# Performance work log

Measured on AMD Instinct MI355X. Metric: run time of the kernel, lower is better.

Reference implementation:

```python
import jax, jax.numpy as jnp
import numpy as np

SXY_BF, SC_BF = 70.0, 12.0
COMPAT_BF, COMPAT_SPATIAL = 4.0, 2.0
SXY_SPATIAL = 6
NUM_ITER = 5
N_OUT = 21


def _gkern_depthwise(std, chans):
    # matches gkern(): sig_sq even -> r = sig_sq - 1, s = 2r+1
    sig_sq = std ** 2
    r = sig_sq if sig_sq % 2 else sig_sq - 1
    s = 2 * r + 1
    yy, xx = np.meshgrid(np.arange(s), np.arange(s), indexing='ij')
    k = np.exp(-(((yy - r) ** 2 + (xx - r) ** 2) / (2.0 * sig_sq)))
    k = k / k.sum()
    # original builds a [C,C,s,s] diagonal kernel == depthwise [C,1,s,s]
    return jnp.asarray(np.broadcast_to(k[None, None], (chans, 1, s, s)).copy(), jnp.float32)


def setup_inputs() -> dict:
    key = jax.random.key(0)
    k1, k2 = jax.random.split(key)
    unary = jax.random.uniform(k1, (2, N_OUT, 64, 64), dtype=jnp.float32)
    ref = jax.random.uniform(k2, (2, 3, 64, 64), dtype=jnp.float32) * 255.0  # RGB image
    gk = _gkern_depthwise(SXY_SPATIAL, N_OUT)
    kstd = jnp.asarray([SXY_BF, SXY_BF, SC_BF, SC_BF, SC_BF], jnp.float32)
    return {"unary": unary, "ref": ref, "gk": gk, "kstd": kstd}


def _crf_forward(unary, ref, gk, kstd):
    N, C, H, W = unary.shape
    P = H * W
    # stacked reference features: [y, x, r, g, b]
    yy, xx = jnp.meshgrid(jnp.arange(H, dtype=jnp.float32),
                          jnp.arange(W, dtype=jnp.float32), indexing='ij')
    grid = jnp.broadcast_to(jnp.stack([yy, xx])[None], (N, 2, H, W))
    stacked = jnp.concatenate([grid, ref], axis=1)  # [N,5,H,W]
    feats = (stacked / kstd[None, :, None, None]).reshape(N, -1, P).transpose(0, 2, 1)  # [N,P,5]
    # exact dense Gaussian (bilateral) kernel: K[p,q] = exp(-||f_p - f_q||^2 / 2)
    sq = jnp.sum(feats * feats, axis=-1)  # [N,P]
    d2 = sq[:, :, None] + sq[:, None, :] - 2.0 * jnp.einsum('npd,nqd->npq', feats, feats)
    K = jnp.exp(-0.5 * jnp.maximum(d2, 0.0))  # [N,P,P]

    U = jnp.log(jnp.clip(unary, 1e-5, 1.0))
    q = jax.nn.softmax(U, axis=1)
    pad = gk.shape[-1] // 2
    for i in range(NUM_ITER):
        qbf = jnp.einsum('npq,ncq->ncp', K, q.reshape(N, C, P)).reshape(N, C, H, W)
        qsf = jax.lax.conv_general_dilated(
            q, gk, window_strides=(1, 1), padding=[(pad, pad), (pad, pad)],
            feature_group_count=C, dimension_numbers=('NCHW', 'OIHW', 'NCHW'))
        q_hat = U + COMPAT_BF * qbf + COMPAT_SPATIAL * qsf
        q = jax.nn.softmax(q_hat, axis=1)  # normalize_final_iter=True
    return q


def reference(unary, ref, gk, kstd):
    return _crf_forward(unary, ref, gk, kstd)
```

## Files before the change

kernel.cpp:

```cpp
#include <hip/hip_runtime.h>
#include <math.h>

#ifndef __has_builtin
#define __has_builtin(x) 0
#endif
#if __has_builtin(__builtin_amdgcn_exp2f)
#define EXP2F(x) __builtin_amdgcn_exp2f(x)
#else
#define EXP2F(x) exp2f(x)
#endif

#define L2E  1.44269504088896340736f
#define RL2E 0.69314718055994530942f

#define NBATCH 2
#define NC 21
#define NP 4096
#define KR 35
#define NUM_ITER 5

typedef _Float16 half_t;
typedef _Float16 h8 __attribute__((ext_vector_type(8)));
typedef _Float16 h4 __attribute__((ext_vector_type(4)));
typedef float f4 __attribute__((ext_vector_type(4)));
typedef float f2 __attribute__((ext_vector_type(2)));
#define MFMA16(a, b, c) __builtin_amdgcn_mfma_f32_16x16x32_f16((a), (b), (c), 0, 0, 0)

static __device__ __forceinline__ f2 pk_fma(f2 a, f2 b, f2 c) {
    f2 d;
    asm volatile("v_pk_fma_f32 %0, %1, %2, %3" : "=v"(d) : "v"(a), "v"(b), "v"(c));
    return d;
}
static __device__ __forceinline__ f2 pk_add(f2 a, f2 b) {
    f2 d;
    asm volatile("v_pk_add_f32 %0, %1, %2" : "=v"(d) : "v"(a), "v"(b));
    return d;
}

#define PTILE 128
#define NPT   32
#define SQ    16
#define CHUNK 256
#define STEPS 8
#define NBBIL (NBATCH * NPT * SQ)
#define NBCONV (NBATCH * NC)
#define SEG_HALVES 256

#define OFF_QFEAT 0
#define OFF_QSOA  65536
#define OFF_UT    114688
#define OFF_QSF   311296
#define OFF_G     483328
#define OFF_QH16  485376
#define OFF_PART  845824
#define OFF_KMAT  2942976

#define LDS_BYTES 27648
#define QLS_STRIDE 264

__global__ __launch_bounds__(256) void setup_kernel(
    const float* __restrict__ unary, const float* __restrict__ ref,
    const float* __restrict__ kstd, float* __restrict__ ws,
    float* __restrict__ outq)
{
    int gid = blockIdx.x * 256 + threadIdx.x;
    if (gid < 4096) {
        float s = 0.f;
        for (int t = -KR; t <= KR; ++t) s += expf(-(float)(t * t) * (1.0f / 72.0f));
        int y = gid >> 6, yp = gid & 63;
        int d = y - yp;
        float v = (d >= -KR && d <= KR) ? expf(-(float)(d * d) * (1.0f / 72.0f)) / s : 0.f;
        ((half_t*)(ws + OFF_G))[gid] = (half_t)v;
    }
    if (gid >= NBATCH * NP) return;
    int n = gid >> 12, p = gid & (NP - 1);
    int y = p >> 6, x = p & 63;
    float k0 = kstd[0], k1 = kstd[1], k2 = kstd[2], k3 = kstd[3], k4 = kstd[4];
    const float* rp = ref + n * 3 * NP + p;
    float f0 = (float)y / k0;
    float f1 = (float)x / k1;
    float f2_ = rp[0]      / k2;
    float f3 = rp[NP]     / k3;
    float f4_ = rp[2 * NP] / k4;
    float sq = f0*f0 + f1*f1 + f2_*f2_ + f3*f3 + f4_*f4_;
    float h  = -0.5f * L2E * sq;
    float* qf = ws + OFF_QFEAT + gid * 8;
    qf[0]=L2E*f0; qf[1]=L2E*f1; qf[2]=L2E*f2_; qf[3]=L2E*f3; qf[4]=L2E*f4_;
    qf[5]=h; qf[6]=0.f; qf[7]=0.f;
    float* qs = ws + OFF_QSOA;
    qs[0*8192 + gid] = L2E*f0;  qs[1*8192 + gid] = L2E*f1;
    qs[2*8192 + gid] = L2E*f2_; qs[3*8192 + gid] = L2E*f3;
    qs[4*8192 + gid] = L2E*f4_; qs[5*8192 + gid] = h;

    float U[NC], e[NC];
    const float* up = unary + n * NC * NP + p;
    float m = -1e30f;
    for (int c = 0; c < NC; ++c) {
        float u = up[c * NP];
        u = fminf(fmaxf(u, 1e-5f), 1.0f);
        U[c] = logf(u);
        m = fmaxf(m, U[c]);
    }
    float ssum = 0.f;
    for (int c = 0; c < NC; ++c) { e[c] = EXP2F(L2E * (U[c] - m)); ssum += e[c]; }
    float inv = 1.0f / ssum;
    float* ut = ws + OFF_UT + gid * 24;
    half_t* qh = (half_t*)(ws + OFF_QH16);
    for (int c = 0; c < NC; ++c) {
        float qv = e[c] * inv;
        ut[c] = U[c];
        qh[(n * 24 + c) * NP + p] = (half_t)qv;
        outq[(n * NC + c) * NP + p] = qv;
    }
    ut[21] = 0.f; ut[22] = 0.f; ut[23] = 0.f;
    qh[(n * 24 + 21) * NP + p] = (half_t)0.f;
    qh[(n * 24 + 22) * NP + p] = (half_t)0.f;
    qh[(n * 24 + 23) * NP + p] = (half_t)0.f;
}

__global__ __launch_bounds__(256) void bilat_conv_kernel(
    const float* __restrict__ qfeatA,
    const float* __restrict__ qsoa,
    const half_t* __restrict__ qh16,
    const half_t* __restrict__ gmat,
    half_t* __restrict__ part,
    float* __restrict__ qsf,
    half_t* __restrict__ kmat,
    int first)
{
    __shared__ __align__(16) char lds[LDS_BYTES];
    int b = blockIdx.x;
    int tid = threadIdx.x;
    int l = tid & 63, w = tid >> 6;

    if (b < NBBIL) {
        int n  = b & 1;
        int pt = (b >> 1) & (NPT - 1);
        int s  = b >> 6;
        float*  qsoaS = (float*)lds;
        half_t* qls   = (half_t*)(lds + 6144);

        if (first) {
            for (int i = tid; i < 6 * (CHUNK / 4); i += 256) {
                int d = i >> 6, g = i & 63;
                *(f4*)(qsoaS + d * CHUNK + g * 4) =
                    *(const f4*)(qsoa + (size_t)d * 8192 + n * NP + s * CHUNK + g * 4);
            }
        }
        for (int i = tid; i < 21 * (CHUNK / 8); i += 256) {
            int c = i >> 5, g = i & 31;
            *(h8*)(qls + c * QLS_STRIDE + g * 8) =
                *(const h8*)(qh16 + (size_t)(n * 24 + c) * NP + s * CHUNK + g * 8);
        }
        for (int i = tid; i < 11 * 33; i += 256) {
            int c = 21 + i / 33, g = i % 33;
            *(h8*)(qls + c * QLS_STRIDE + g * 8) = (h8)(half_t)0.f;
        }
        half_t* kbase = kmat + (size_t)((b * 4 + w) * 2) * 8 * 512 + (size_t)l * 8;

        f4 acc[2][2];
        #pragma unroll
        for (int mt = 0; mt < 2; ++mt) { acc[mt][0] = (f4)0.f; acc[mt][1] = (f4)0.f; }
        int kq = (l >> 4) * 8;

        if (first) {
            f2 pf2[2][5], ph2[2];
            #pragma unroll
            for (int mt = 0; mt < 2; ++mt) {
                const float* fp = qfeatA + (size_t)(n * NP + pt * PTILE + (w * 2 + mt) * 16 + (l & 15)) * 8;
                #pragma unroll
                for (int i = 0; i < 5; ++i) {
                    float v = fp[i] * RL2E;
                    pf2[mt][i] = (f2){v, v};
                }
                ph2[mt] = (f2){fp[5], fp[5]};
            }
            __syncthreads();

            for (int step = 0; step < STEPS; ++step) {
                int qbase = step * 32 + kq;
                h8 kv[2];
                #pragma unroll
                for (int hf = 0; hf < 2; ++hf) {
                    f4 qf0 = *(const f4*)(qsoaS + 0 * CHUNK + qbase + hf * 4);
                    f4 qf1 = *(const f4*)(qsoaS + 1 * CHUNK + qbase + hf * 4);
                    f4 qf2 = *(const f4*)(qsoaS + 2 * CHUNK + qbase + hf * 4);
                    f4 qf3 = *(const f4*)(qsoaS + 3 * CHUNK + qbase + hf * 4);
                    f4 qf4 = *(const f4*)(qsoaS + 4 * CHUNK + qbase + hf * 4);
                    f4 qf5 = *(const f4*)(qsoaS + 5 * CHUNK + qbase + hf * 4);
                    #pragma unroll
                    for (int pr = 0; pr < 2; ++pr) {
                        f2 q0 = {qf0[2*pr], qf0[2*pr+1]};
                        f2 q1 = {qf1[2*pr], qf1[2*pr+1]};
                        f2 q2 = {qf2[2*pr], qf2[2*pr+1]};
                        f2 q3 = {qf3[2*pr], qf3[2*pr+1]};
                        f2 q4 = {qf4[2*pr], qf4[2*pr+1]};
                        f2 qh2 = {qf5[2*pr], qf5[2*pr+1]};
                        #pragma unroll
                        for (int mt = 0; mt < 2; ++mt) {
                            f2 e = pk_add(qh2, ph2[mt]);
                            e = pk_fma(pf2[mt][0], q0, e);
                            e = pk_fma(pf2[mt][1], q1, e);
                            e = pk_fma(pf2[mt][2], q2, e);
                            e = pk_fma(pf2[mt][3], q3, e);
                            e = pk_fma(pf2[mt][4], q4, e);
                            kv[mt][hf * 4 + pr * 2]     = (half_t)EXP2F(e[0]);
                            kv[mt][hf * 4 + pr * 2 + 1] = (half_t)EXP2F(e[1]);
                        }
                    }
                }
                *(h8*)(kbase + (size_t)(0 * 8 + step) * 512) = kv[0];
                *(h8*)(kbase + (size_t)(1 * 8 + step) * 512) = kv[1];

                h8 bf0 = *(const h8*)(qls + (size_t)(l & 15) * QLS_STRIDE + qbase);
                h8 bf1 = *(const h8*)(qls + (size_t)(16 + (l & 15)) * QLS_STRIDE + qbase);
                #pragma unroll
                for (int mt = 0; mt < 2; ++mt) {
                    acc[mt][0] = MFMA16(kv[mt], bf0, acc[mt][0]);
                    acc[mt][1] = MFMA16(kv[mt], bf1, acc[mt][1]);
                }
            }
        } else {
            __syncthreads();
            #pragma unroll
            for (int step = 0; step < STEPS; ++step) {
                int qbase = step * 32 + kq;
                h8 kv0 = *(const h8*)(kbase + (size_t)(0 * 8 + step) * 512);
                h8 kv1 = *(const h8*)(kbase + (size_t)(1 * 8 + step) * 512);
                h8 bf0 = *(const h8*)(qls + (size_t)(l & 15) * QLS_STRIDE + qbase);
                h8 bf1 = *(const h8*)(qls + (size_t)(16 + (l & 15)) * QLS_STRIDE + qbase);
                acc[0][0] = MFMA16(kv0, bf0, acc[0][0]);
                acc[0][1] = MFMA16(kv0, bf1, acc[0][1]);
                acc[1][0] = MFMA16(kv1, bf0, acc[1][0]);
                acc[1][1] = MFMA16(kv1, bf1, acc[1][1]);
            }
        }
        #pragma unroll
        for (int mt = 0; mt < 2; ++mt) {
            #pragma unroll
            for (int cht = 0; cht < 2; ++cht) {
                int segFlat = ((((s * 2 + n) * NPT + pt) * 4 + w) * 2 + mt) * 2 + cht;
                h4 hv;
                hv[0] = (half_t)acc[mt][cht][0];
                hv[1] = (half_t)acc[mt][cht][1];
                hv[2] = (half_t)acc[mt][cht][2];
                hv[3] = (half_t)acc[mt][cht][3];
                *(h4*)(part + (size_t)segFlat * SEG_HALVES + l * 4) = hv;
            }
        }
    } else {
        int cb = b - NBBIL;
        int n = cb / NC, c = cb % NC;
        half_t* qt = (half_t*)lds;
        half_t* gl = (half_t*)(lds + 9216);
        half_t* dl = (half_t*)(lds + 18432);

        for (int i = tid; i < 512; i += 256) {
            int row = i >> 3, g = i & 7;
            *(h8*)(gl + row * 72 + g * 8) = *(const h8*)(gmat + row * 64 + g * 8);
        }
        const half_t* qsrc = qh16 + (size_t)(n * 24 + c) * NP;
        for (int i = tid; i < 512; i += 256) {
            int row = i >> 3, g = i & 7;
            h8 v = *(const h8*)(qsrc + row * 64 + g * 8);
            #pragma unroll
            for (int k = 0; k < 8; ++k) qt[(g * 8 + k) * 72 + row] = v[k];
        }
        __syncthreads();

        int m0 = w * 16;
        f4 acc1[4];
        #pragma unroll
        for (int nt = 0; nt < 4; ++nt) acc1[nt] = (f4)0.f;
        #pragma unroll
        for (int ks = 0; ks < 2; ++ks) {
            h8 af = *(const h8*)(gl + (size_t)(m0 + (l & 15)) * 72 + ks * 32 + (l >> 4) * 8);
            #pragma unroll
            for (int nt = 0; nt < 4; ++nt) {
                h8 bf = *(const h8*)(qt + (size_t)(nt * 16 + (l & 15)) * 72 + ks * 32 + (l >> 4) * 8);
                acc1[nt] = MFMA16(af, bf, acc1[nt]);
            }
        }
        #pragma unroll
        for (int nt = 0; nt < 4; ++nt)
            #pragma unroll
            for (int r = 0; r < 4; ++r)
                dl[(size_t)(m0 + (l >> 4) * 4 + r) * 72 + nt * 16 + (l & 15)] = (half_t)acc1[nt][r];
        __syncthreads();

        f4 acc2[4];
        #pragma unroll
        for (int nt = 0; nt < 4; ++nt) acc2[nt] = (f4)0.f;
        #pragma unroll
        for (int ks = 0; ks < 2; ++ks) {
            h8 af = *(const h8*)(dl + (size_t)(m0 + (l & 15)) * 72 + ks * 32 + (l >> 4) * 8);
            #pragma unroll
            for (int nt = 0; nt < 4; ++nt) {
                h8 bf = *(const h8*)(gl + (size_t)(nt * 16 + (l & 15)) * 72 + ks * 32 + (l >> 4) * 8);
                acc2[nt] = MFMA16(af, bf, acc2[nt]);
            }
        }
        float* dst = qsf + (size_t)(n * NC + c) * NP;
        #pragma unroll
        for (int nt = 0; nt < 4; ++nt)
            #pragma unroll
            for (int r = 0; r < 4; ++r)
                dst[(size_t)(m0 + (l >> 4) * 4 + r) * 64 + nt * 16 + (l & 15)] = acc2[nt][r];
    }
}

__global__ __launch_bounds__(256) void reduce_update_kernel(
    const half_t* __restrict__ part, const float* __restrict__ ut_,
    const float* __restrict__ qsf, float* __restrict__ outq,
    half_t* __restrict__ qh16, int last)
{
    __shared__ float red[1024];
    int rb = blockIdx.x;
    int tid = threadIdx.x;
    int n = rb & 1, pt = (rb >> 1) & 31, wq = rb >> 6;
    int lseg = tid >> 6, l = tid & 63;

    float a0 = 0.f, a1 = 0.f, a2 = 0.f, a3 = 0.f;
    for (int s = 0; s < SQ; ++s) {
        size_t segF = (size_t)((((s * 2 + n) * NPT + pt) * 4 + wq) * 4 + lseg);
        h4 v = *(const h4*)(part + segF * SEG_HALVES + (size_t)l * 4);
        a0 += (float)v[0]; a1 += (float)v[1]; a2 += (float)v[2]; a3 += (float)v[3];
    }
    *(f4*)(red + tid * 4) = (f4){a0, a1, a2, a3};
    __syncthreads();

    if (tid < 32) {
        int pp = tid;
        int p = pt * PTILE + wq * 32 + pp;
        int gid = n * NP + p;
        int mtl = pp >> 4, mrow = pp & 15;
        int lg2 = mrow >> 2, reg = mrow & 3;

        const float* ut = ut_ + (size_t)gid * 24;
        const float* qs = qsf + (size_t)n * NC * NP + p;
        float e[NC];
        float m = -1e30f;
        #pragma unroll
        for (int c = 0; c < NC; ++c) {
            int cht = c >> 4, chL = c & 15;
            float qb = red[(mtl * 2 + cht) * 256 + (lg2 * 16 + chL) * 4 + reg];
            float li = ut[c] + 4.0f * qb + 2.0f * qs[c * NP];
            e[c] = li;
            m = fmaxf(m, li);
        }
        float ssum = 0.f;
        #pragma unroll
        for (int c = 0; c < NC; ++c) { float v = EXP2F(L2E * (e[c] - m)); e[c] = v; ssum += v; }
        float inv = 1.0f / ssum;
        if (last) {
            #pragma unroll
            for (int c = 0; c < NC; ++c)
                outq[(size_t)(n * NC + c) * NP + p] = e[c] * inv;
        } else {
            #pragma unroll
            for (int c = 0; c < NC; ++c)
                qh16[(size_t)(n * 24 + c) * NP + p] = (half_t)(e[c] * inv);
        }
    }
}

extern "C" void kernel_launch(void* const* d_in, const int* in_sizes, int n_in,
                              void* d_out, int out_size, void* d_ws, size_t ws_size,
                              hipStream_t stream)
{
    const float* unary = (const float*)d_in[0];
    const float* ref   = (const float*)d_in[1];
    const float* kstd  = (const float*)d_in[3];
    float* ws   = (float*)d_ws;
    float* outq = (float*)d_out;

    const float*  qfeatA = ws + OFF_QFEAT;
    const float*  qsoa   = ws + OFF_QSOA;
    float*        ut     = ws + OFF_UT;
    float*        qsf    = ws + OFF_QSF;
    const half_t* gmat   = (const half_t*)(ws + OFF_G);
    half_t*       qh16   = (half_t*)(ws + OFF_QH16);
    half_t*       part   = (half_t*)(ws + OFF_PART);
    half_t*       kmat   = (half_t*)(ws + OFF_KMAT);

    setup_kernel<<<32, 256, 0, stream>>>(unary, ref, kstd, ws, outq);
    for (int it = 0; it < NUM_ITER; ++it) {
        bilat_conv_kernel<<<NBBIL + NBCONV, 256, 0, stream>>>(
            qfeatA, qsoa, qh16, gmat, part, qsf, kmat, it == 0 ? 1 : 0);
        reduce_update_kernel<<<256, 256, 0, stream>>>(
            part, ut, qsf, outq, qh16, it == NUM_ITER - 1 ? 1 : 0);
    }
}
```

Measured before the change: 159.2 us.

## Fold spatial Gaussian into combined dense kernel and fuse reduction into one iteration kernel

Folds the separable spatial Gaussian convolution into the dense bilateral matrix, so each stored kernel entry holds 4*K_bf + 2*G_spatial. The conv blocks and the separate partial-sum reduction kernel go away. Each block now owns 32 pixels across all 4096 columns, with 512 threads and double-buffered LDS chunks, and reduces across waves in LDS before doing the softmax. This cuts launches from two per iteration to one and removes the fp16 partial round trip. The cost is less parallelism, since only 256 blocks each loop 16 chunks serially. The combined values are also stored in fp16, which may cost precision.

```diff
diff --git a/kernel.cpp b/kernel.cpp
--- a/kernel.cpp
+++ b/kernel.cpp
@@ -12,16 +12,17 @@
 
 #define L2E  1.44269504088896340736f
 #define RL2E 0.69314718055994530942f
+#define GEXPC (-L2E / 72.0f)
 
 #define NBATCH 2
 #define NC 21
 #define NP 4096
 #define KR 35
 #define NUM_ITER 5
+#define CHUNK 256
 
 typedef _Float16 half_t;
 typedef _Float16 h8 __attribute__((ext_vector_type(8)));
-typedef _Float16 h4 __attribute__((ext_vector_type(4)));
 typedef float f4 __attribute__((ext_vector_type(4)));
 typedef float f2 __attribute__((ext_vector_type(2)));
 #define MFMA16(a, b, c) __builtin_amdgcn_mfma_f32_16x16x32_f16((a), (b), (c), 0, 0, 0)
@@ -37,40 +38,25 @@
     return d;
 }
 
-#define PTILE 128
-#define NPT   32
-#define SQ    16
-#define CHUNK 256
-#define STEPS 8
-#define NBBIL (NBATCH * NPT * SQ)
-#define NBCONV (NBATCH * NC)
-#define SEG_HALVES 256
-
 #define OFF_QFEAT 0
 #define OFF_QSOA  65536
 #define OFF_UT    114688
-#define OFF_QSF   311296
-#define OFF_G     483328
-#define OFF_QH16  485376
-#define OFF_PART  845824
-#define OFF_KMAT  2942976
-
-#define LDS_BYTES 27648
+#define OFF_QA    311296
+#define OFF_QB    409600
+#define OFF_G     507904
+#define OFF_KMAT  524288
+
 #define QLS_STRIDE 264
 
 __global__ __launch_bounds__(256) void setup_kernel(
     const float* __restrict__ unary, const float* __restrict__ ref,
-    const float* __restrict__ kstd, float* __restrict__ ws,
-    float* __restrict__ outq)
+    const float* __restrict__ kstd, float* __restrict__ ws)
 {
     int gid = blockIdx.x * 256 + threadIdx.x;
-    if (gid < 4096) {
+    if (gid == 0) {
         float s = 0.f;
         for (int t = -KR; t <= KR; ++t) s += expf(-(float)(t * t) * (1.0f / 72.0f));
-        int y = gid >> 6, yp = gid & 63;
-        int d = y - yp;
-        float v = (d >= -KR && d <= KR) ? expf(-(float)(d * d) * (1.0f / 72.0f)) / s : 0.f;
-        ((half_t*)(ws + OFF_G))[gid] = (half_t)v;
+        ws[OFF_G] = 1.0f - 2.0f * log2f(s);
     }
     if (gid >= NBATCH * NP) return;
     int n = gid >> 12, p = gid & (NP - 1);
@@ -105,252 +91,208 @@
     for (int c = 0; c < NC; ++c) { e[c] = EXP2F(L2E * (U[c] - m)); ssum += e[c]; }
     float inv = 1.0f / ssum;
     float* ut = ws + OFF_UT + gid * 24;
-    half_t* qh = (half_t*)(ws + OFF_QH16);
+    half_t* qh = (half_t*)(ws + OFF_QA);
     for (int c = 0; c < NC; ++c) {
         float qv = e[c] * inv;
         ut[c] = U[c];
         qh[(n * 24 + c) * NP + p] = (half_t)qv;
-        outq[(n * NC + c) * NP + p] = qv;
-    }
-    ut[21] = 0.f; ut[22] = 0.f; ut[23] = 0.f;
-    qh[(n * 24 + 21) * NP + p] = (half_t)0.f;
-    qh[(n * 24 + 22) * NP + p] = (half_t)0.f;
-    qh[(n * 24 + 23) * NP + p] = (half_t)0.f;
-}
-
-__global__ __launch_bounds__(256) void bilat_conv_kernel(
+    }
+}
+
+__global__ __launch_bounds__(512) void crf_iter_kernel(
     const float* __restrict__ qfeatA,
     const float* __restrict__ qsoa,
-    const half_t* __restrict__ qh16,
-    const half_t* __restrict__ gmat,
-    half_t* __restrict__ part,
-    float* __restrict__ qsf,
+    const half_t* __restrict__ qin,
+    half_t* __restrict__ qout,
+    const float* __restrict__ ut_,
     half_t* __restrict__ kmat,
-    int first)
+    float* __restrict__ outq,
+    const float* __restrict__ gconst,
+    int first, int last)
 {
-    __shared__ __align__(16) char lds[LDS_BYTES];
+    __shared__ __align__(16) char lds[46080];
+    half_t* qlsA = (half_t*)lds;
+    half_t* qlsB = (half_t*)(lds + 16896);
+    float*  qsoA = (float*)(lds + 33792);
+    float*  qsoB = (float*)(lds + 39936);
+
     int b = blockIdx.x;
+    int n = b & 1, ptA = b >> 1;
     int tid = threadIdx.x;
-    int l = tid & 63, w = tid >> 6;
-
-    if (b < NBBIL) {
-        int n  = b & 1;
-        int pt = (b >> 1) & (NPT - 1);
-        int s  = b >> 6;
-        float*  qsoaS = (float*)lds;
-        half_t* qls   = (half_t*)(lds + 6144);
-
+    int l = tid & 63, v = tid >> 6;
+    int kq = (l >> 4) * 8;
+    int qoff = v * 32 + kq;
+
+    for (int i = tid; i < 2 * 363; i += 512) {
+        int bi = (i >= 363);
+        int j = i - bi * 363;
+        int c = 21 + j / 33, g = j % 33;
+        half_t* q = bi ? qlsB : qlsA;
+        *(h8*)(q + c * QLS_STRIDE + g * 8) = (h8)(half_t)0.f;
+    }
+    for (int i = tid; i < 672; i += 512) {
+        int c = i >> 5, g = i & 31;
+        *(h8*)(qlsA + c * QLS_STRIDE + g * 8) =
+            *(const h8*)(qin + (size_t)(n * 24 + c) * NP + g * 8);
+    }
+    if (first) {
+        for (int i = tid; i < 384; i += 512) {
+            int d = i >> 6, g = i & 63;
+            *(f4*)(qsoA + d * CHUNK + g * 4) =
+                *(const f4*)(qsoa + (size_t)d * 8192 + n * NP + g * 4);
+        }
+    }
+
+    f2 pf2[2][5], ph2[2];
+    int yp[2] = {0, 0}, xp[2] = {0, 0};
+    float C2p1 = 0.f;
+    if (first) {
+        C2p1 = gconst[0];
+        #pragma unroll
+        for (int mt = 0; mt < 2; ++mt) {
+            int pp = ptA * 32 + mt * 16 + (l & 15);
+            const float* fp = qfeatA + (size_t)(n * NP + pp) * 8;
+            #pragma unroll
+            for (int i = 0; i < 5; ++i) { float vv = fp[i] * RL2E; pf2[mt][i] = (f2){vv, vv}; }
+            ph2[mt] = (f2){fp[5], fp[5]};
+            yp[mt] = pp >> 6; xp[mt] = pp & 63;
+        }
+    }
+
+    f4 acc[2][2];
+    acc[0][0] = (f4)0.f; acc[0][1] = (f4)0.f;
+    acc[1][0] = (f4)0.f; acc[1][1] = (f4)0.f;
+
+    size_t fb = (size_t)b * (16 * 16 * 512);
+    h8 kv0 = (h8)(half_t)0.f, kv1 = (h8)(half_t)0.f;
+    if (!first) {
+        kv0 = *(const h8*)(kmat + fb + (size_t)(v * 2 + 0) * 512 + l * 8);
+        kv1 = *(const h8*)(kmat + fb + (size_t)(v * 2 + 1) * 512 + l * 8);
+    }
+    __syncthreads();
+
+    for (int s = 0; s < 16; ++s) {
+        half_t* qc = (s & 1) ? qlsB : qlsA;
+        half_t* qn = (s & 1) ? qlsA : qlsB;
+        float*  sc = (s & 1) ? qsoB : qsoA;
+        float*  sn = (s & 1) ? qsoA : qsoB;
+
+        if (s < 15) {
+            for (int i = tid; i < 672; i += 512) {
+                int c = i >> 5, g = i & 31;
+                *(h8*)(qn + c * QLS_STRIDE + g * 8) =
+                    *(const h8*)(qin + (size_t)(n * 24 + c) * NP + (s + 1) * CHUNK + g * 8);
+            }
+            if (first) {
+                for (int i = tid; i < 384; i += 512) {
+                    int d = i >> 6, g = i & 63;
+                    *(f4*)(sn + d * CHUNK + g * 4) =
+                        *(const f4*)(qsoa + (size_t)d * 8192 + n * NP + (s + 1) * CHUNK + g * 4);
+                }
+            }
+        }
+
+        h8 kvc0, kvc1;
         if (first) {
-            for (int i = tid; i < 6 * (CHUNK / 4); i += 256) {
-                int d = i >> 6, g = i & 63;
-                *(f4*)(qsoaS + d * CHUNK + g * 4) =
-                    *(const f4*)(qsoa + (size_t)d * 8192 + n * NP + s * CHUNK + g * 4);
-            }
-        }
-        for (int i = tid; i < 21 * (CHUNK / 8); i += 256) {
-            int c = i >> 5, g = i & 31;
-            *(h8*)(qls + c * QLS_STRIDE + g * 8) =
-                *(const h8*)(qh16 + (size_t)(n * 24 + c) * NP + s * CHUNK + g * 8);
-        }
-        for (int i = tid; i < 11 * 33; i += 256) {
-            int c = 21 + i / 33, g = i % 33;
-            *(h8*)(qls + c * QLS_STRIDE + g * 8) = (h8)(half_t)0.f;
-        }
-        half_t* kbase = kmat + (size_t)((b * 4 + w) * 2) * 8 * 512 + (size_t)l * 8;
-
-        f4 acc[2][2];
-        #pragma unroll
-        for (int mt = 0; mt < 2; ++mt) { acc[mt][0] = (f4)0.f; acc[mt][1] = (f4)0.f; }
-        int kq = (l >> 4) * 8;
-
-        if (first) {
-            f2 pf2[2][5], ph2[2];
+            h8 kv[2];
             #pragma unroll
-            for (int mt = 0; mt < 2; ++mt) {
-                const float* fp = qfeatA + (size_t)(n * NP + pt * PTILE + (w * 2 + mt) * 16 + (l & 15)) * 8;
+            for (int hf = 0; hf < 2; ++hf) {
+                f4 qf0 = *(const f4*)(sc + 0 * CHUNK + qoff + hf * 4);
+                f4 qf1 = *(const f4*)(sc + 1 * CHUNK + qoff + hf * 4);
+                f4 qf2 = *(const f4*)(sc + 2 * CHUNK + qoff + hf * 4);
+                f4 qf3 = *(const f4*)(sc + 3 * CHUNK + qoff + hf * 4);
+                f4 qf4 = *(const f4*)(sc + 4 * CHUNK + qoff + hf * 4);
+                f4 qf5 = *(const f4*)(sc + 5 * CHUNK + qoff + hf * 4);
                 #pragma unroll
-                for (int i = 0; i < 5; ++i) {
-                    float v = fp[i] * RL2E;
-                    pf2[mt][i] = (f2){v, v};
-                }
-                ph2[mt] = (f2){fp[5], fp[5]};
-            }
-            __syncthreads();
-
-            for (int step = 0; step < STEPS; ++step) {
-                int qbase = step * 32 + kq;
-                h8 kv[2];
-                #pragma unroll
-                for (int hf = 0; hf < 2; ++hf) {
-                    f4 qf0 = *(const f4*)(qsoaS + 0 * CHUNK + qbase + hf * 4);
-                    f4 qf1 = *(const f4*)(qsoaS + 1 * CHUNK + qbase + hf * 4);
-                    f4 qf2 = *(const f4*)(qsoaS + 2 * CHUNK + qbase + hf * 4);
-                    f4 qf3 = *(const f4*)(qsoaS + 3 * CHUNK + qbase + hf * 4);
-                    f4 qf4 = *(const f4*)(qsoaS + 4 * CHUNK + qbase + hf * 4);
-                    f4 qf5 = *(const f4*)(qsoaS + 5 * CHUNK + qbase + hf * 4);
+                for (int pr = 0; pr < 2; ++pr) {
+                    f2 q0 = {qf0[2*pr], qf0[2*pr+1]};
+                    f2 q1 = {qf1[2*pr], qf1[2*pr+1]};
+                    f2 q2 = {qf2[2*pr], qf2[2*pr+1]};
+                    f2 q3 = {qf3[2*pr], qf3[2*pr+1]};
+                    f2 q4 = {qf4[2*pr], qf4[2*pr+1]};
+                    f2 qh2 = {qf5[2*pr], qf5[2*pr+1]};
                     #pragma unroll
-                    for (int pr = 0; pr < 2; ++pr) {
-                        f2 q0 = {qf0[2*pr], qf0[2*pr+1]};
-                        f2 q1 = {qf1[2*pr], qf1[2*pr+1]};
-                        f2 q2 = {qf2[2*pr], qf2[2*pr+1]};
-                        f2 q3 = {qf3[2*pr], qf3[2*pr+1]};
-                        f2 q4 = {qf4[2*pr], qf4[2*pr+1]};
-                        f2 qh2 = {qf5[2*pr], qf5[2*pr+1]};
+                    for (int mt = 0; mt < 2; ++mt) {
+                        f2 e = pk_add(qh2, ph2[mt]);
+                        e = pk_fma(pf2[mt][0], q0, e);
+                        e = pk_fma(pf2[mt][1], q1, e);
+                        e = pk_fma(pf2[mt][2], q2, e);
+                        e = pk_fma(pf2[mt][3], q3, e);
+                        e = pk_fma(pf2[mt][4], q4, e);
                         #pragma unroll
-                        for (int mt = 0; mt < 2; ++mt) {
-                            f2 e = pk_add(qh2, ph2[mt]);
-                            e = pk_fma(pf2[mt][0], q0, e);
-                            e = pk_fma(pf2[mt][1], q1, e);
-                            e = pk_fma(pf2[mt][2], q2, e);
-                            e = pk_fma(pf2[mt][3], q3, e);
-                            e = pk_fma(pf2[mt][4], q4, e);
-                            kv[mt][hf * 4 + pr * 2]     = (half_t)EXP2F(e[0]);
-                            kv[mt][hf * 4 + pr * 2 + 1] = (half_t)EXP2F(e[1]);
+                        for (int jj = 0; jj < 2; ++jj) {
+                            int qpix = s * CHUNK + qoff + hf * 4 + pr * 2 + jj;
+                            int dy = yp[mt] - (qpix >> 6);
+                            int dx = xp[mt] - (qpix & 63);
+                            float ge = 0.f;
+                            if ((unsigned)(dy + KR) <= 2u * KR && (unsigned)(dx + KR) <= 2u * KR)
+                                ge = EXP2F((float)(dy * dy + dx * dx) * GEXPC + C2p1);
+                            float mval = EXP2F(e[jj] + 2.0f) + ge;
+                            kv[mt][hf * 4 + pr * 2 + jj] = (half_t)mval;
                         }
                     }
                 }
-                *(h8*)(kbase + (size_t)(0 * 8 + step) * 512) = kv[0];
-                *(h8*)(kbase + (size_t)(1 * 8 + step) * 512) = kv[1];
-
-                h8 bf0 = *(const h8*)(qls + (size_t)(l & 15) * QLS_STRIDE + qbase);
-                h8 bf1 = *(const h8*)(qls + (size_t)(16 + (l & 15)) * QLS_STRIDE + qbase);
-                #pragma unroll
-                for (int mt = 0; mt < 2; ++mt) {
-                    acc[mt][0] = MFMA16(kv[mt], bf0, acc[mt][0]);
-                    acc[mt][1] = MFMA16(kv[mt], bf1, acc[mt][1]);
-                }
             }
+            kvc0 = kv[0]; kvc1 = kv[1];
+            *(h8*)(kmat + fb + (size_t)(s * 16 + v * 2 + 0) * 512 + l * 8) = kvc0;
+            *(h8*)(kmat + fb + (size_t)(s * 16 + v * 2 + 1) * 512 + l * 8) = kvc1;
         } else {
-            __syncthreads();
-            #pragma unroll
-            for (int step = 0; step < STEPS; ++step) {
-                int qbase = step * 32 + kq;
-                h8 kv0 = *(const h8*)(kbase + (size_t)(0 * 8 + step) * 512);
-                h8 kv1 = *(const h8*)(kbase + (size_t)(1 * 8 + step) * 512);
-                h8 bf0 = *(const h8*)(qls + (size_t)(l & 15) * QLS_STRIDE + qbase);
-                h8 bf1 = *(const h8*)(qls + (size_t)(16 + (l & 15)) * QLS_STRIDE + qbase);
-                acc[0][0] = MFMA16(kv0, bf0, acc[0][0]);
-                acc[0][1] = MFMA16(kv0, bf1, acc[0][1]);
-                acc[1][0] = MFMA16(kv1, bf0, acc[1][0]);
-                acc[1][1] = MFMA16(kv1, bf1, acc[1][1]);
+            kvc0 = kv0; kvc1 = kv1;
+            if (s < 15) {
+                kv0 = *(const h8*)(kmat + fb + (size_t)((s + 1) * 16 + v * 2 + 0) * 512 + l * 8);
+                kv1 = *(const h8*)(kmat + fb + (size_t)((s + 1) * 16 + v * 2 + 1) * 512 + l * 8);
             }
         }
-        #pragma unroll
-        for (int mt = 0; mt < 2; ++mt) {
-            #pragma unroll
-            for (int cht = 0; cht < 2; ++cht) {
-                int segFlat = ((((s * 2 + n) * NPT + pt) * 4 + w) * 2 + mt) * 2 + cht;
-                h4 hv;
-                hv[0] = (half_t)acc[mt][cht][0];
-                hv[1] = (half_t)acc[mt][cht][1];
-                hv[2] = (half_t)acc[mt][cht][2];
-                hv[3] = (half_t)acc[mt][cht][3];
-                *(h4*)(part + (size_t)segFlat * SEG_HALVES + l * 4) = hv;
-            }
-        }
-    } else {
-        int cb = b - NBBIL;
-        int n = cb / NC, c = cb % NC;
-        half_t* qt = (half_t*)lds;
-        half_t* gl = (half_t*)(lds + 9216);
-        half_t* dl = (half_t*)(lds + 18432);
-
-        for (int i = tid; i < 512; i += 256) {
-            int row = i >> 3, g = i & 7;
-            *(h8*)(gl + row * 72 + g * 8) = *(const h8*)(gmat + row * 64 + g * 8);
-        }
-        const half_t* qsrc = qh16 + (size_t)(n * 24 + c) * NP;
-        for (int i = tid; i < 512; i += 256) {
-            int row = i >> 3, g = i & 7;
-            h8 v = *(const h8*)(qsrc + row * 64 + g * 8);
-            #pragma unroll
-            for (int k = 0; k < 8; ++k) qt[(g * 8 + k) * 72 + row] = v[k];
-        }
+
+        h8 bf0 = *(const h8*)(qc + (size_t)(l & 15) * QLS_STRIDE + qoff);
+        h8 bf1 = *(const h8*)(qc + (size_t)(16 + (l & 15)) * QLS_STRIDE + qoff);
+        acc[0][0] = MFMA16(kvc0, bf0, acc[0][0]);
+        acc[0][1] = MFMA16(kvc0, bf1, acc[0][1]);
+        acc[1][0] = MFMA16(kvc1, bf0, acc[1][0]);
+        acc[1][1] = MFMA16(kvc1, bf1, acc[1][1]);
         __syncthreads();
-
-        int m0 = w * 16;
-        f4 acc1[4];
-        #pragma unroll
-        for (int nt = 0; nt < 4; ++nt) acc1[nt] = (f4)0.f;
-        #pragma unroll
-        for (int ks = 0; ks < 2; ++ks) {
-            h8 af = *(const h8*)(gl + (size_t)(m0 + (l & 15)) * 72 + ks * 32 + (l >> 4) * 8);
-            #pragma unroll
-            for (int nt = 0; nt < 4; ++nt) {
-                h8 bf = *(const h8*)(qt + (size_t)(nt * 16 + (l & 15)) * 72 + ks * 32 + (l >> 4) * 8);
-                acc1[nt] = MFMA16(af, bf, acc1[nt]);
-            }
-        }
-        #pragma unroll
-        for (int nt = 0; nt < 4; ++nt)
-            #pragma unroll
-            for (int r = 0; r < 4; ++r)
-                dl[(size_t)(m0 + (l >> 4) * 4 + r) * 72 + nt * 16 + (l & 15)] = (half_t)acc1[nt][r];
-        __syncthreads();
-
-        f4 acc2[4];
-        #pragma unroll
-        for (int nt = 0; nt < 4; ++nt) acc2[nt] = (f4)0.f;
-        #pragma unroll
-        for (int ks = 0; ks < 2; ++ks) {
-            h8 af = *(const h8*)(dl + (size_t)(m0 + (l & 15)) * 72 + ks * 32 + (l >> 4) * 8);
-            #pragma unroll
-            for (int nt = 0; nt < 4; ++nt) {
-                h8 bf = *(const h8*)(gl + (size_t)(nt * 16 + (l & 15)) * 72 + ks * 32 + (l >> 4) * 8);
-                acc2[nt] = MFMA16(af, bf, acc2[nt]);
-            }
-        }
-        float* dst = qsf + (size_t)(n * NC + c) * NP;
-        #pragma unroll
-        for (int nt = 0; nt < 4; ++nt)
-            #pragma unroll
-            for (int r = 0; r < 4; ++r)
-                dst[(size_t)(m0 + (l >> 4) * 4 + r) * 64 + nt * 16 + (l & 15)] = acc2[nt][r];
-    }
-}
-
-__global__ __launch_bounds__(256) void reduce_update_kernel(
-    const half_t* __restrict__ part, const float* __restrict__ ut_,
-    const float* __restrict__ qsf, float* __restrict__ outq,
-    half_t* __restrict__ qh16, int last)
-{
-    __shared__ float red[1024];
-    int rb = blockIdx.x;
-    int tid = threadIdx.x;
-    int n = rb & 1, pt = (rb >> 1) & 31, wq = rb >> 6;
-    int lseg = tid >> 6, l = tid & 63;
-
-    float a0 = 0.f, a1 = 0.f, a2 = 0.f, a3 = 0.f;
-    for (int s = 0; s < SQ; ++s) {
-        size_t segF = (size_t)((((s * 2 + n) * NPT + pt) * 4 + wq) * 4 + lseg);
-        h4 v = *(const h4*)(part + segF * SEG_HALVES + (size_t)l * 4);
-        a0 += (float)v[0]; a1 += (float)v[1]; a2 += (float)v[2]; a3 += (float)v[3];
-    }
-    *(f4*)(red + tid * 4) = (f4){a0, a1, a2, a3};
+    }
+
+    f4* redf = (f4*)lds;
+    #pragma unroll
+    for (int mt = 0; mt < 2; ++mt)
+        #pragma unroll
+        for (int cht = 0; cht < 2; ++cht)
+            redf[(size_t)(v * 4 + mt * 2 + cht) * 64 + l] = acc[mt][cht];
     __syncthreads();
 
+    f4* red2 = (f4*)(lds + 33792);
+    if (tid < 256) {
+        int mc = tid >> 6, ll = tid & 63;
+        f4 sum = redf[(size_t)(0 * 4 + mc) * 64 + ll];
+        #pragma unroll
+        for (int vv = 1; vv < 8; ++vv)
+            sum = sum + redf[(size_t)(vv * 4 + mc) * 64 + ll];
+        red2[mc * 64 + ll] = sum;
+    }
+    __syncthreads();
+
     if (tid < 32) {
-        int pp = tid;
-        int p = pt * PTILE + wq * 32 + pp;
+        int pl = tid;
+        int p = ptA * 32 + pl;
         int gid = n * NP + p;
-        int mtl = pp >> 4, mrow = pp & 15;
-        int lg2 = mrow >> 2, reg = mrow & 3;
-
+        int mt = pl >> 4, prow = pl & 15;
+        int lg = prow >> 2, reg = prow & 3;
         const float* ut = ut_ + (size_t)gid * 24;
-        const float* qs = qsf + (size_t)n * NC * NP + p;
+        const float* r2 = (const float*)red2;
         float e[NC];
         float m = -1e30f;
         #pragma unroll
         for (int c = 0; c < NC; ++c) {
             int cht = c >> 4, chL = c & 15;
-            float qb = red[(mtl * 2 + cht) * 256 + (lg2 * 16 + chL) * 4 + reg];
-            float li = ut[c] + 4.0f * qb + 2.0f * qs[c * NP];
+            float qb = r2[((mt * 2 + cht) * 64 + (lg * 16 + chL)) * 4 + reg];
+            float li = ut[c] + qb;
             e[c] = li;
             m = fmaxf(m, li);
         }
         float ssum = 0.f;
         #pragma unroll
-        for (int c = 0; c < NC; ++c) { float v = EXP2F(L2E * (e[c] - m)); e[c] = v; ssum += v; }
+        for (int c = 0; c < NC; ++c) { float vv = EXP2F(L2E * (e[c] - m)); e[c] = vv; ssum += vv; }
         float inv = 1.0f / ssum;
         if (last) {
             #pragma unroll
@@ -359,7 +301,7 @@
         } else {
             #pragma unroll
             for (int c = 0; c < NC; ++c)
-                qh16[(size_t)(n * 24 + c) * NP + p] = (half_t)(e[c] * inv);
+                qout[(size_t)(n * 24 + c) * NP + p] = (half_t)(e[c] * inv);
         }
     }
 }
@@ -374,20 +316,20 @@
     float* ws   = (float*)d_ws;
     float* outq = (float*)d_out;
 
-    const float*  qfeatA = ws + OFF_QFEAT;
-    const float*  qsoa   = ws + OFF_QSOA;
-    float*        ut     = ws + OFF_UT;
-    float*        qsf    = ws + OFF_QSF;
-    const half_t* gmat   = (const half_t*)(ws + OFF_G);
-    half_t*       qh16   = (half_t*)(ws + OFF_QH16);
-    half_t*       part   = (half_t*)(ws + OFF_PART);
-    half_t*       kmat   = (half_t*)(ws + OFF_KMAT);
-
-    setup_kernel<<<32, 256, 0, stream>>>(unary, ref, kstd, ws, outq);
+    const float* qfeatA = ws + OFF_QFEAT;
+    const float* qsoa   = ws + OFF_QSOA;
+    const float* ut     = ws + OFF_UT;
+    half_t* qA   = (half_t*)(ws + OFF_QA);
+    half_t* qB   = (half_t*)(ws + OFF_QB);
+    const float* gconst = ws + OFF_G;
+    half_t* kmat = (half_t*)(ws + OFF_KMAT);
+
+    setup_kernel<<<32, 256, 0, stream>>>(unary, ref, kstd, ws);
     for (int it = 0; it < NUM_ITER; ++it) {
-        bilat_conv_kernel<<<NBBIL + NBCONV, 256, 0, stream>>>(
-            qfeatA, qsoa, qh16, gmat, part, qsf, kmat, it == 0 ? 1 : 0);
-        reduce_update_kernel<<<256, 256, 0, stream>>>(
-            part, ut, qsf, outq, qh16, it == NUM_ITER - 1 ? 1 : 0);
-    }
-}
+        half_t* qin  = (it & 1) ? qB : qA;
+        half_t* qout = (it & 1) ? qA : qB;
+        crf_iter_kernel<<<NBATCH * 128, 512, 0, stream>>>(
+            qfeatA, qsoa, qin, qout, ut, kmat, outq, gconst,
+            it == 0 ? 1 : 0, it == NUM_ITER - 1 ? 1 : 0);
+    }
+}
```

Result: slower. 185.8 us (+16.7%).
